# Kernel tuning notes

Hardware: AMD Instinct MI355X
Metric: run time of the kernel (lower is better)

Reference implementation:

```python
import jax, jax.numpy as jnp
import numpy as np

NBLOCK = 2000
DIM = 2048
B, T = 32, 1024
EPS = 1e-12  # F.normalize eps


def _l2norm(v, axis):
    n = jnp.sqrt(jnp.sum(v * v, axis=axis, keepdims=True))
    return v / jnp.maximum(n, EPS)


def setup_inputs() -> dict:
    key = jax.random.key(0)
    kx, km, kw = jax.random.split(key, 3)
    x = jax.random.normal(kx, (B, T, DIM), dtype=jnp.float32)
    mask = jax.random.randint(km, (B, T), 0, 2).astype(jnp.int32)
    stdv = 1.0 / np.sqrt(DIM)
    weight = jax.random.uniform(kw, (NBLOCK, DIM), dtype=jnp.float32,
                                minval=-stdv, maxval=stdv)
    return {"x": x, "mask": mask, "weight": weight}


def reference(x, mask, weight):
    half = x.shape[0] // 2
    nblock = weight.shape[0]
    m = mask.astype(x.dtype)  # [B, T]

    # diversity: || W W^T - I ||_F
    gram = weight @ weight.T  # [N, N]
    diversity_loss = jnp.linalg.norm(gram - jnp.eye(nblock, dtype=weight.dtype))

    # cosine-similarity attention: [B, T, N]
    att = jnp.einsum('btd,nd->btn', _l2norm(x, axis=2), _l2norm(weight, axis=1))

    # uniformity loss: masked sum over T, softmax over blocks, mean over half-batch
    s = jnp.einsum('btn,bt->nb', att[:half], m[:half])  # [N, half]
    tmp = jnp.mean(jax.nn.softmax(s, axis=0), axis=1)   # [N]
    u_loss = jnp.linalg.norm(tmp)

    # per-row min over masked positions of the top-1 similarity
    top1 = jnp.max(att, axis=2)  # [B, T] (only topk[...,0] is used)
    inf = jnp.asarray(jnp.inf, dtype=x.dtype)
    masked_top1 = jnp.where(m > 0, top1, inf)
    min_sim = jnp.min(masked_top1[:half], axis=1)   # [half]
    ab_min = jnp.min(masked_top1[half:], axis=1)    # [half]

    return (0.2 * diversity_loss,
            2.0 - jnp.mean(min_sim) + jnp.mean(ab_min),
            0.5 * u_loss)
```

## Files before the change

kernel.cpp:

```cpp
#include <hip/hip_runtime.h>

typedef unsigned char u8;
typedef unsigned short u16;
typedef unsigned int u32;
typedef __attribute__((ext_vector_type(8))) short short8;
typedef __attribute__((ext_vector_type(4))) u16 ushort4_t;
typedef __attribute__((ext_vector_type(4))) float fx4;
typedef __attribute__((ext_vector_type(8))) int int8v;

#define DIMK 2048
#define NBLK 2000
#define SCL 32.0f
#define SCLBYTE 0x7A7A7A7A

typedef const __attribute__((address_space(1))) void* gp_t;
typedef __attribute__((address_space(3))) void* lp_t;

__device__ __forceinline__ u16 f2bf(float f) {
  u32 u = __float_as_uint(f);
  u32 r = (u + 0x7fffu + ((u >> 16) & 1u)) >> 16;
  return (u16)r;
}

__device__ __forceinline__ u32 pk4_fp8(float a, float b, float c, float d) {
  int v = 0;
  v = __builtin_amdgcn_cvt_pk_fp8_f32(a, b, v, false);
  v = __builtin_amdgcn_cvt_pk_fp8_f32(c, d, v, true);
  return (u32)v;
}

__device__ __forceinline__ u32 fkey(float f) {
  u32 u = __float_as_uint(f);
  return (u & 0x80000000u) ? ~u : (u | 0x80000000u);
}
__device__ __forceinline__ float dekey(u32 k) {
  u32 u = (k & 0x80000000u) ? (k ^ 0x80000000u) : ~k;
  return __uint_as_float(u);
}

__device__ __forceinline__ void gemm_tile(const u16* __restrict__ Abase,
                                          const u16* __restrict__ Bbase,
                                          int row0, int col0,
                                          u16* lsA, u16* lsB,
                                          fx4 acc[4][4])
{
  const int tid  = threadIdx.x;
  const int wv   = tid >> 6;
  const int lane = tid & 63;
  const int wr   = wv & 1, wc = wv >> 1;
  const int quad = lane >> 4, lc = lane & 15;

  const int srow = wv * 32 + (lane >> 2);
  const int skel = (((lane & 3) ^ ((lane >> 3) & 3)) * 8);
  const u16* gA0 = Abase + (size_t)(row0 + srow) * DIMK + skel;
  const u16* gA1 = gA0 + (size_t)16 * DIMK;
  const u16* gB0 = Bbase + (size_t)(col0 + srow) * DIMK + skel;
  const u16* gB1 = gB0 + (size_t)16 * DIMK;
  u16* lA0 = lsA + wv * 1024;
  u16* lA1 = lsA + wv * 1024 + 512;
  u16* lB0 = lsB + wv * 1024;
  u16* lB1 = lsB + wv * 1024 + 512;

  const int fIntra = lc * 32 + ((quad ^ ((lc >> 1) & 3)) * 8);

#pragma unroll
  for (int mi = 0; mi < 4; mi++)
#pragma unroll
    for (int ni = 0; ni < 4; ni++)
      acc[mi][ni] = fx4{0.f, 0.f, 0.f, 0.f};

  for (int k0 = 0; k0 < DIMK; k0 += 32) {
    __syncthreads();
    __builtin_amdgcn_global_load_lds((gp_t)gA0, (lp_t)lA0, 16, 0, 0);
    __builtin_amdgcn_global_load_lds((gp_t)gA1, (lp_t)lA1, 16, 0, 0);
    __builtin_amdgcn_global_load_lds((gp_t)gB0, (lp_t)lB0, 16, 0, 0);
    __builtin_amdgcn_global_load_lds((gp_t)gB1, (lp_t)lB1, 16, 0, 0);
    gA0 += 32; gA1 += 32; gB0 += 32; gB1 += 32;
    __syncthreads();
    short8 af[4], bfr[4];
#pragma unroll
    for (int mi = 0; mi < 4; mi++)
      af[mi] = *(const short8*)(lsA + (wr * 4 + mi) * 512 + fIntra);
#pragma unroll
    for (int ni = 0; ni < 4; ni++)
      bfr[ni] = *(const short8*)(lsB + (wc * 4 + ni) * 512 + fIntra);
#pragma unroll
    for (int mi = 0; mi < 4; mi++)
#pragma unroll
      for (int ni = 0; ni < 4; ni++)
        acc[mi][ni] = __builtin_amdgcn_mfma_f32_16x16x32_bf16(af[mi], bfr[ni], acc[mi][ni], 0, 0, 0);
  }
}

__global__ __launch_bounds__(256) void norm_rows_x(const float* __restrict__ x,
                                                   u8* __restrict__ Xq)
{
  const int wv = threadIdx.x >> 6, lane = threadIdx.x & 63;
  const int row = blockIdx.x * 4 + wv;
  const float4* xr = (const float4*)(x + (size_t)row * DIMK);
  float4 v[8];
  float ss = 0.f;
#pragma unroll
  for (int j = 0; j < 8; j++) {
    v[j] = xr[j * 64 + lane];
    ss += v[j].x*v[j].x + v[j].y*v[j].y + v[j].z*v[j].z + v[j].w*v[j].w;
  }
#pragma unroll
  for (int off = 1; off < 64; off <<= 1) ss += __shfl_xor(ss, off);
  float inv = SCL / fmaxf(sqrtf(ss), 1e-12f);
  u32* o = (u32*)(Xq + (size_t)row * DIMK);
#pragma unroll
  for (int j = 0; j < 8; j++)
    o[j * 64 + lane] = pk4_fp8(v[j].x * inv, v[j].y * inv, v[j].z * inv, v[j].w * inv);
}

__global__ __launch_bounds__(256) void norm_rows_w(const float* __restrict__ w,
                                                   u8* __restrict__ Wq,
                                                   u16* __restrict__ Wb)
{
  const int wv = threadIdx.x >> 6, lane = threadIdx.x & 63;
  const int row = blockIdx.x * 4 + wv;
  u32* oq = (u32*)(Wq + (size_t)row * DIMK);
  ushort4_t* ob_ = (ushort4_t*)(Wb + (size_t)row * DIMK);
  if (row < NBLK) {
    const float4* wr_ = (const float4*)(w + (size_t)row * DIMK);
    float4 v[8];
    float ss = 0.f;
#pragma unroll
    for (int j = 0; j < 8; j++) {
      v[j] = wr_[j * 64 + lane];
      ss += v[j].x*v[j].x + v[j].y*v[j].y + v[j].z*v[j].z + v[j].w*v[j].w;
    }
#pragma unroll
    for (int off = 1; off < 64; off <<= 1) ss += __shfl_xor(ss, off);
    float inv = SCL / fmaxf(sqrtf(ss), 1e-12f);
#pragma unroll
    for (int j = 0; j < 8; j++) {
      oq[j * 64 + lane] = pk4_fp8(v[j].x * inv, v[j].y * inv, v[j].z * inv, v[j].w * inv);
      ushort4_t tb;
      tb[0] = f2bf(v[j].x); tb[1] = f2bf(v[j].y);
      tb[2] = f2bf(v[j].z); tb[3] = f2bf(v[j].w);
      ob_[j * 64 + lane] = tb;
    }
  } else {
    ushort4_t z = ushort4_t{0, 0, 0, 0};
#pragma unroll
    for (int j = 0; j < 8; j++) { oq[j * 64 + lane] = 0u; ob_[j * 64 + lane] = z; }
  }
}

__global__ __launch_bounds__(256) void gram_kernel(const u16* __restrict__ Wb,
                                                   float* __restrict__ divsum)
{
  __shared__ __align__(16) u16 lsA[4096];
  __shared__ __align__(16) u16 lsB[4096];
  fx4 acc[4][4];
  const int i0 = blockIdx.y * 128, j0 = blockIdx.x * 128;
  gemm_tile(Wb, Wb, i0, j0, lsA, lsB, acc);
  const int tid = threadIdx.x, wv = tid >> 6, lane = tid & 63;
  const int wr = wv & 1, wc = wv >> 1, quad = lane >> 4, lc = lane & 15;
  float local = 0.f;
#pragma unroll
  for (int mi = 0; mi < 4; mi++) {
#pragma unroll
    for (int ni = 0; ni < 4; ni++) {
#pragma unroll
      for (int r = 0; r < 4; r++) {
        int i = i0 + wr * 64 + mi * 16 + quad * 4 + r;
        int j = j0 + wc * 64 + ni * 16 + lc;
        float g = acc[mi][ni][r];
        float d = (i == j && i < NBLK) ? 1.0f : 0.0f;
        float e = g - d;
        local += e * e;
      }
    }
  }
#pragma unroll
  for (int off = 1; off < 64; off <<= 1) local += __shfl_xor(local, off);
  if (lane == 0) atomicAdd(divsum, local);
}

__global__ __launch_bounds__(256) void att_kernel(const u8* __restrict__ Xq,
                                                  const u8* __restrict__ Wq,
                                                  const int* __restrict__ mask,
                                                  u32* __restrict__ top1k,
                                                  float* __restrict__ s)
{
  __shared__ __align__(32) u8 lsA[16384];
  __shared__ __align__(32) u8 lsB[16384];
  __shared__ float sMask[128];
  const int xb = blockIdx.x, yb = blockIdx.y;
  const int tid = threadIdx.x;
  if (tid < 128) sMask[tid] = (float)mask[yb * 128 + tid];
  const int wv = tid >> 6, lane = tid & 63;
  const int wr = wv & 1, wc = wv >> 1, quad = lane >> 4, lc = lane & 15;

  const int csrc = (lane & 7) ^ (((lane >> 4) & 3) << 1);
  const u8* gA = Xq + (size_t)(yb * 128 + wv * 32 + (lane >> 3)) * DIMK + csrc * 16;
  const u8* gB = Wq + (size_t)(xb * 128 + wv * 32 + (lane >> 3)) * DIMK + csrc * 16;
  u8* lA = lsA + wv * 4096;
  u8* lB = lsB + wv * 4096;

  const int fIntra = lc * 128 + ((quad ^ ((lc >> 1) & 3)) << 5);
  const int fA = (wr * 4) * 2048 + fIntra;
  const int fB = (wc * 4) * 2048 + fIntra;

  fx4 acc[4][4];
#pragma unroll
  for (int mi = 0; mi < 4; mi++)
#pragma unroll
    for (int ni = 0; ni < 4; ni++)
      acc[mi][ni] = fx4{0.f, 0.f, 0.f, 0.f};

  for (int k0 = 0; k0 < 16; k0++) {
    __syncthreads();
#pragma unroll
    for (int i = 0; i < 4; i++) {
      __builtin_amdgcn_global_load_lds((gp_t)(gA + (size_t)i * 8 * DIMK), (lp_t)(lA + i * 1024), 16, 0, 0);
      __builtin_amdgcn_global_load_lds((gp_t)(gB + (size_t)i * 8 * DIMK), (lp_t)(lB + i * 1024), 16, 0, 0);
    }
    gA += 128; gB += 128;
    __syncthreads();
    int8v af[4], bq[4];
#pragma unroll
    for (int mi = 0; mi < 4; mi++)
      af[mi] = *(const int8v*)(lsA + fA + mi * 2048);
#pragma unroll
    for (int ni = 0; ni < 4; ni++)
      bq[ni] = *(const int8v*)(lsB + fB + ni * 2048);
#pragma unroll
    for (int mi = 0; mi < 4; mi++)
#pragma unroll
      for (int ni = 0; ni < 4; ni++)
        acc[mi][ni] = __builtin_amdgcn_mfma_scale_f32_16x16x128_f8f6f4(
            af[mi], bq[ni], acc[mi][ni], 0, 0, 0, SCLBYTE, 0, SCLBYTE);
  }

  const int colbase = xb * 128 + wc * 64;

#pragma unroll
  for (int mi = 0; mi < 4; mi++) {
#pragma unroll
    for (int r = 0; r < 4; r++) {
      float v = -3.0e38f;
#pragma unroll
      for (int ni = 0; ni < 4; ni++) {
        int col = colbase + ni * 16 + lc;
        float av = acc[mi][ni][r];
        v = (col < NBLK && av > v) ? av : v;
      }
      v = fmaxf(v, __shfl_xor(v, 1));
      v = fmaxf(v, __shfl_xor(v, 2));
      v = fmaxf(v, __shfl_xor(v, 4));
      v = fmaxf(v, __shfl_xor(v, 8));
      if (lc == 0) {
        int row = yb * 128 + wr * 64 + mi * 16 + quad * 4 + r;
        atomicMax(&top1k[row], fkey(v));
      }
    }
  }

  if (yb < 128) {
    const int b = yb >> 3;
#pragma unroll
    for (int ni = 0; ni < 4; ni++) {
      float sv = 0.f;
#pragma unroll
      for (int mi = 0; mi < 4; mi++) {
#pragma unroll
        for (int r = 0; r < 4; r++)
          sv += sMask[wr * 64 + mi * 16 + quad * 4 + r] * acc[mi][ni][r];
      }
      sv += __shfl_xor(sv, 16);
      sv += __shfl_xor(sv, 32);
      int col = colbase + ni * 16 + lc;
      if (quad == 0 && col < NBLK)
        atomicAdd(&s[b * 2048 + col], sv);
    }
  }
}

__global__ __launch_bounds__(256) void softmax_kernel(const float* __restrict__ s,
                                                      float* __restrict__ tmp)
{
  const int b = blockIdx.x, tid = threadIdx.x;
  const float* sb = s + b * 2048;
  __shared__ float red[4];
  float mx = -3.0e38f;
  for (int n = tid; n < NBLK; n += 256) mx = fmaxf(mx, sb[n]);
#pragma unroll
  for (int off = 1; off < 64; off <<= 1) mx = fmaxf(mx, __shfl_xor(mx, off));
  if ((tid & 63) == 0) red[tid >> 6] = mx;
  __syncthreads();
  mx = fmaxf(fmaxf(red[0], red[1]), fmaxf(red[2], red[3]));
  __syncthreads();
  float se = 0.f;
  for (int n = tid; n < NBLK; n += 256) se += expf(sb[n] - mx);
#pragma unroll
  for (int off = 1; off < 64; off <<= 1) se += __shfl_xor(se, off);
  if ((tid & 63) == 0) red[tid >> 6] = se;
  __syncthreads();
  se = red[0] + red[1] + red[2] + red[3];
  float scale = 1.0f / (se * 16.0f);
  for (int n = tid; n < NBLK; n += 256) atomicAdd(&tmp[n], expf(sb[n] - mx) * scale);
}

__global__ __launch_bounds__(1024) void finalize_kernel(const u32* __restrict__ top1k,
                                                        const int* __restrict__ mask,
                                                        const float* __restrict__ tmp,
                                                        const float* __restrict__ divsum,
                                                        float* __restrict__ out)
{
  const int tid = threadIdx.x;
  __shared__ float sMin[32];
  __shared__ float sSq[16];
  const int b = tid >> 5, li = tid & 31;
  float mn = 3.0e38f;
  for (int t = li; t < 1024; t += 32) {
    int idx = b * 1024 + t;
    if (mask[idx] > 0) mn = fminf(mn, dekey(top1k[idx]));
  }
#pragma unroll
  for (int off = 1; off < 32; off <<= 1) mn = fminf(mn, __shfl_xor(mn, off));
  if (li == 0) sMin[b] = mn;
  float ssq = 0.f;
  for (int n = tid; n < NBLK; n += 1024) { float v = tmp[n]; ssq += v * v; }
#pragma unroll
  for (int off = 1; off < 64; off <<= 1) ssq += __shfl_xor(ssq, off);
  if ((tid & 63) == 0) sSq[tid >> 6] = ssq;
  __syncthreads();
  if (tid == 0) {
    float m0 = 0.f, m1 = 0.f;
    for (int i = 0; i < 16; i++) { m0 += sMin[i]; m1 += sMin[16 + i]; }
    m0 *= (1.0f / 16.0f); m1 *= (1.0f / 16.0f);
    float sq = 0.f;
    for (int i = 0; i < 16; i++) sq += sSq[i];
    out[0] = 0.2f * sqrtf(divsum[0]);
    out[1] = 2.0f - m0 + m1;
    out[2] = 0.5f * sqrtf(sq);
  }
}

extern "C" void kernel_launch(void* const* d_in, const int* in_sizes, int n_in,
                              void* d_out, int out_size, void* d_ws, size_t ws_size,
                              hipStream_t stream) {
  const float* x    = (const float*)d_in[0];
  const int*   mask = (const int*)d_in[1];
  const float* w    = (const float*)d_in[2];
  float* out = (float*)d_out;

  char* ws = (char*)d_ws;
  u32*   top1k  = (u32*)(ws);
  float* s      = (float*)(ws + 131072);
  float* tmp    = (float*)(ws + 262144);
  float* divsum = (float*)(ws + 270336);
  u8*    Xq     = (u8*)(ws + 270592);
  u8*    Wq     = (u8*)(ws + 270592 + 67108864ull);
  u16*   Wb     = (u16*)(ws + 270592 + 67108864ull + 4194304ull);

  hipMemsetAsync(ws, 0, 270592, stream);

  norm_rows_w<<<dim3(512), dim3(256), 0, stream>>>(w, Wq, Wb);
  norm_rows_x<<<dim3(8192), dim3(256), 0, stream>>>(x, Xq);
  gram_kernel<<<dim3(16, 16), dim3(256), 0, stream>>>(Wb, divsum);
  att_kernel<<<dim3(16, 256), dim3(256), 0, stream>>>(Xq, Wq, mask, top1k, s);
  softmax_kernel<<<dim3(16), dim3(256), 0, stream>>>(s, tmp);
  finalize_kernel<<<dim3(1), dim3(1024), 0, stream>>>(top1k, mask, tmp, divsum, out);
}
```

Baseline: 867.0 us.

## Switch attention GEMM to 32x32x64 FP8 MFMA with 64-byte K tiles

Replaces the 16x16x128 scaled FP8 MFMA in the attention kernel with the 32x32x64 variant. Each wave now holds a 2x2 grid of 32x32 accumulators instead of 4x4 of 16x16. The K step is halved to 64 bytes, which shrinks LDS to 8 KB per operand and doubles the loop iterations. LDS swizzling, fragment loads and the epilogue row/column mapping for top-1 and masked sums are rewritten to match the new layout. The larger MFMA shape issues fewer instructions and reuses operands better, but twice as many barriers and smaller loads per iteration may expose more memory latency.

```diff
diff --git a/kernel.cpp b/kernel.cpp
--- a/kernel.cpp
+++ b/kernel.cpp
@@ -6,6 +6,8 @@
 typedef __attribute__((ext_vector_type(8))) short short8;
 typedef __attribute__((ext_vector_type(4))) u16 ushort4_t;
 typedef __attribute__((ext_vector_type(4))) float fx4;
+typedef __attribute__((ext_vector_type(16))) float fx16;
+typedef __attribute__((ext_vector_type(4))) int int4v;
 typedef __attribute__((ext_vector_type(8))) int int8v;
 
 #define DIMK 2048
@@ -186,75 +188,86 @@
                                                   u32* __restrict__ top1k,
                                                   float* __restrict__ s)
 {
-  __shared__ __align__(32) u8 lsA[16384];
-  __shared__ __align__(32) u8 lsB[16384];
+  __shared__ __align__(32) u8 lsA[8192];
+  __shared__ __align__(32) u8 lsB[8192];
   __shared__ float sMask[128];
   const int xb = blockIdx.x, yb = blockIdx.y;
   const int tid = threadIdx.x;
   if (tid < 128) sMask[tid] = (float)mask[yb * 128 + tid];
   const int wv = tid >> 6, lane = tid & 63;
-  const int wr = wv & 1, wc = wv >> 1, quad = lane >> 4, lc = lane & 15;
-
-  const int csrc = (lane & 7) ^ (((lane >> 4) & 3) << 1);
-  const u8* gA = Xq + (size_t)(yb * 128 + wv * 32 + (lane >> 3)) * DIMK + csrc * 16;
-  const u8* gB = Wq + (size_t)(xb * 128 + wv * 32 + (lane >> 3)) * DIMK + csrc * 16;
-  u8* lA = lsA + wv * 4096;
-  u8* lB = lsB + wv * 4096;
-
-  const int fIntra = lc * 128 + ((quad ^ ((lc >> 1) & 3)) << 5);
-  const int fA = (wr * 4) * 2048 + fIntra;
-  const int fB = (wc * 4) * 2048 + fIntra;
-
-  fx4 acc[4][4];
-#pragma unroll
-  for (int mi = 0; mi < 4; mi++)
-#pragma unroll
-    for (int ni = 0; ni < 4; ni++)
-      acc[mi][ni] = fx4{0.f, 0.f, 0.f, 0.f};
-
-  for (int k0 = 0; k0 < 16; k0++) {
+  const int wr = wv & 1, wc = wv >> 1;
+  const int h = lane >> 5, cl = lane & 31;
+
+  const int csrc = (lane & 3) ^ ((lane >> 3) & 3);
+  const u8* gA = Xq + (size_t)(yb * 128 + wv * 32 + (lane >> 2)) * DIMK + csrc * 16;
+  const u8* gB = Wq + (size_t)(xb * 128 + wv * 32 + (lane >> 2)) * DIMK + csrc * 16;
+  u8* lA = lsA + wv * 2048;
+  u8* lB = lsB + wv * 2048;
+
+  const int rsw = (lane >> 1) & 3;
+  const int f0 = cl * 64 + (((2 * h) ^ rsw) << 4);
+  const int f1 = cl * 64 + (((2 * h + 1) ^ rsw) << 4);
+
+  fx16 acc[2][2];
+#pragma unroll
+  for (int mi = 0; mi < 2; mi++)
+#pragma unroll
+    for (int ni = 0; ni < 2; ni++)
+#pragma unroll
+      for (int r = 0; r < 16; r++)
+        acc[mi][ni][r] = 0.f;
+
+  for (int k0 = 0; k0 < 32; k0++) {
     __syncthreads();
-#pragma unroll
-    for (int i = 0; i < 4; i++) {
-      __builtin_amdgcn_global_load_lds((gp_t)(gA + (size_t)i * 8 * DIMK), (lp_t)(lA + i * 1024), 16, 0, 0);
-      __builtin_amdgcn_global_load_lds((gp_t)(gB + (size_t)i * 8 * DIMK), (lp_t)(lB + i * 1024), 16, 0, 0);
-    }
-    gA += 128; gB += 128;
+    __builtin_amdgcn_global_load_lds((gp_t)gA, (lp_t)lA, 16, 0, 0);
+    __builtin_amdgcn_global_load_lds((gp_t)(gA + (size_t)16 * DIMK), (lp_t)(lA + 1024), 16, 0, 0);
+    __builtin_amdgcn_global_load_lds((gp_t)gB, (lp_t)lB, 16, 0, 0);
+    __builtin_amdgcn_global_load_lds((gp_t)(gB + (size_t)16 * DIMK), (lp_t)(lB + 1024), 16, 0, 0);
+    gA += 64; gB += 64;
     __syncthreads();
-    int8v af[4], bq[4];
-#pragma unroll
-    for (int mi = 0; mi < 4; mi++)
-      af[mi] = *(const int8v*)(lsA + fA + mi * 2048);
-#pragma unroll
-    for (int ni = 0; ni < 4; ni++)
-      bq[ni] = *(const int8v*)(lsB + fB + ni * 2048);
-#pragma unroll
-    for (int mi = 0; mi < 4; mi++)
-#pragma unroll
-      for (int ni = 0; ni < 4; ni++)
-        acc[mi][ni] = __builtin_amdgcn_mfma_scale_f32_16x16x128_f8f6f4(
+    int8v af[2], bq[2];
+#pragma unroll
+    for (int mi = 0; mi < 2; mi++) {
+      const u8* base = lsA + (wr * 2 + mi) * 2048;
+      int4v lo = *(const int4v*)(base + f0);
+      int4v hi = *(const int4v*)(base + f1);
+      af[mi] = int8v{lo[0], lo[1], lo[2], lo[3], hi[0], hi[1], hi[2], hi[3]};
+    }
+#pragma unroll
+    for (int ni = 0; ni < 2; ni++) {
+      const u8* base = lsB + (wc * 2 + ni) * 2048;
+      int4v lo = *(const int4v*)(base + f0);
+      int4v hi = *(const int4v*)(base + f1);
+      bq[ni] = int8v{lo[0], lo[1], lo[2], lo[3], hi[0], hi[1], hi[2], hi[3]};
+    }
+#pragma unroll
+    for (int mi = 0; mi < 2; mi++)
+#pragma unroll
+      for (int ni = 0; ni < 2; ni++)
+        acc[mi][ni] = __builtin_amdgcn_mfma_scale_f32_32x32x64_f8f6f4(
             af[mi], bq[ni], acc[mi][ni], 0, 0, 0, SCLBYTE, 0, SCLBYTE);
   }
 
   const int colbase = xb * 128 + wc * 64;
 
 #pragma unroll
-  for (int mi = 0; mi < 4; mi++) {
-#pragma unroll
-    for (int r = 0; r < 4; r++) {
+  for (int mi = 0; mi < 2; mi++) {
+#pragma unroll
+    for (int reg = 0; reg < 16; reg++) {
       float v = -3.0e38f;
 #pragma unroll
-      for (int ni = 0; ni < 4; ni++) {
-        int col = colbase + ni * 16 + lc;
-        float av = acc[mi][ni][r];
+      for (int ni = 0; ni < 2; ni++) {
+        int col = colbase + ni * 32 + cl;
+        float av = acc[mi][ni][reg];
         v = (col < NBLK && av > v) ? av : v;
       }
       v = fmaxf(v, __shfl_xor(v, 1));
       v = fmaxf(v, __shfl_xor(v, 2));
       v = fmaxf(v, __shfl_xor(v, 4));
       v = fmaxf(v, __shfl_xor(v, 8));
-      if (lc == 0) {
-        int row = yb * 128 + wr * 64 + mi * 16 + quad * 4 + r;
+      v = fmaxf(v, __shfl_xor(v, 16));
+      if (cl == 0) {
+        int row = yb * 128 + wr * 64 + mi * 32 + (reg & 3) + 8 * (reg >> 2) + 4 * h;
         atomicMax(&top1k[row], fkey(v));
       }
     }
@@ -263,18 +276,17 @@
   if (yb < 128) {
     const int b = yb >> 3;
 #pragma unroll
-    for (int ni = 0; ni < 4; ni++) {
+    for (int ni = 0; ni < 2; ni++) {
       float sv = 0.f;
 #pragma unroll
-      for (int mi = 0; mi < 4; mi++) {
-#pragma unroll
-        for (int r = 0; r < 4; r++)
-          sv += sMask[wr * 64 + mi * 16 + quad * 4 + r] * acc[mi][ni][r];
+      for (int mi = 0; mi < 2; mi++) {
+#pragma unroll
+        for (int reg = 0; reg < 16; reg++)
+          sv += sMask[wr * 64 + mi * 32 + (reg & 3) + 8 * (reg >> 2) + 4 * h] * acc[mi][ni][reg];
       }
-      sv += __shfl_xor(sv, 16);
       sv += __shfl_xor(sv, 32);
-      int col = colbase + ni * 16 + lc;
-      if (quad == 0 && col < NBLK)
+      int col = colbase + ni * 32 + cl;
+      if (h == 0 && col < NBLK)
         atomicAdd(&s[b * 2048 + col], sv);
     }
   }
```

Measured after the change: 852.0 us. No clear change (-1.7%).
